# Kernel tuning notes

Measured on AMD Instinct MI355X. Metric: run time of the kernel, lower is better.

Reference implementation:

```python
import jax, jax.numpy as jnp
import numpy as np

D_MODEL = 1024
N_HEADS = 16
D_K = D_MODEL // N_HEADS
D_FF = 4096
EPS = 1e-5


def setup_inputs() -> dict:
    key = jax.random.key(0)
    ks = jax.random.split(key, 12)
    s = 1.0 / np.sqrt(D_MODEL)
    inp = {
        "x": jax.random.normal(ks[0], (2, 2048, D_MODEL), dtype=jnp.float32),
        "Wq": jax.random.normal(ks[1], (D_MODEL, D_MODEL), dtype=jnp.float32) * s,
        "Wk": jax.random.normal(ks[2], (D_MODEL, D_MODEL), dtype=jnp.float32) * s,
        "Wv": jax.random.normal(ks[3], (D_MODEL, D_MODEL), dtype=jnp.float32) * s,
        "Wo": jax.random.normal(ks[4], (D_MODEL, D_MODEL), dtype=jnp.float32) * s,
        "ln1_g": jnp.ones((D_MODEL,), jnp.float32),
        "ln1_b": jnp.zeros((D_MODEL,), jnp.float32),
        "ln2_g": jnp.ones((D_MODEL,), jnp.float32),
        "ln2_b": jnp.zeros((D_MODEL,), jnp.float32),
        "W1": jax.random.normal(ks[5], (D_MODEL, D_FF), dtype=jnp.float32) * s,
        "b1": jnp.zeros((D_FF,), jnp.float32),
        "W2": jax.random.normal(ks[6], (D_FF, D_MODEL), dtype=jnp.float32) * (1.0 / np.sqrt(D_FF)),
        "b2": jnp.zeros((D_MODEL,), jnp.float32),
    }
    return inp


def _layernorm(x, g, b):
    mu = jnp.mean(x, axis=-1, keepdims=True)
    var = jnp.mean(jnp.square(x - mu), axis=-1, keepdims=True)
    return (x - mu) / jnp.sqrt(var + EPS) * g + b


def _mha(x, Wq, Wk, Wv, Wo):
    B, S, D = x.shape
    def split_heads(t):
        return t.reshape(B, S, N_HEADS, D_K).transpose(0, 2, 1, 3)  # [B,H,S,Dk]
    Q = split_heads(x @ Wq)
    K = split_heads(x @ Wk)
    V = split_heads(x @ Wv)
    scores = jnp.einsum("bhsd,bhtd->bhst", Q, K) / np.sqrt(D_K)
    causal = jnp.tril(jnp.ones((S, S), dtype=bool))
    scores = jnp.where(causal, scores, -jnp.inf)
    weights = jax.nn.softmax(scores, axis=-1)
    out = jnp.einsum("bhst,bhtd->bhsd", weights, V)
    out = out.transpose(0, 2, 1, 3).reshape(B, S, D)
    return out @ Wo


def reference(x, Wq, Wk, Wv, Wo, ln1_g, ln1_b, ln2_g, ln2_b, W1, b1, W2, b2):
    # Pre-LN transformer block, dropout in eval mode (identity)
    x = x + _mha(_layernorm(x, ln1_g, ln1_b), Wq, Wk, Wv, Wo)
    h = _layernorm(x, ln2_g, ln2_b)
    ff = jax.nn.gelu(h @ W1 + b1, approximate=False) @ W2 + b2
    return x + ff
```

## Files before the change

kernel.cpp:

```cpp
#include <hip/hip_runtime.h>
#include <cstdint>
#include <cstddef>

#define DEV __device__ __forceinline__

typedef __attribute__((ext_vector_type(8))) __bf16 bf16x8;
typedef __attribute__((ext_vector_type(4))) float f32x4;

typedef const __attribute__((address_space(1))) void gld_gv;
typedef __attribute__((address_space(3))) void gld_sv;

static constexpr int SEQ = 2048, BAT = 2, DM = 1024, DFF = 4096;
static constexpr int MT = BAT * SEQ;
static constexpr float LOG2E = 1.44269504088896340736f;
static constexpr float SM_SHIFT = 16.0f;

struct TrueC  { static constexpr bool value = true;  };
struct FalseC { static constexpr bool value = false; };

DEV unsigned short f2bf_bits(float f) {
    uint32_t u = __builtin_bit_cast(uint32_t, f);
    return (unsigned short)((u + 0x7FFFu + ((u >> 16) & 1u)) >> 16);
}

DEV void gload16(const void* g, void* s) {
    __builtin_amdgcn_global_load_lds((gld_gv*)g, (gld_sv*)s, 16, 0, 0);
}

__global__ __launch_bounds__(256) void wtrans_kernel(const float* __restrict__ W,
        unsigned short* __restrict__ WT, int K, int N, float scale)
{
    __shared__ float tile[64][65];
    const int k0 = blockIdx.x * 64, n0 = blockIdx.y * 64;
    const int t = threadIdx.x, r = t >> 6, c = t & 63;
    #pragma unroll
    for (int p = 0; p < 16; ++p)
        tile[p * 4 + r][c] = W[(size_t)(k0 + p * 4 + r) * N + n0 + c];
    __syncthreads();
    #pragma unroll
    for (int p = 0; p < 16; ++p)
        WT[(size_t)(n0 + p * 4 + r) * K + k0 + c] = f2bf_bits(tile[c][p * 4 + r] * scale);
}

__global__ __launch_bounds__(256) void ln_kernel(const float* __restrict__ x,
        const float* __restrict__ gw, const float* __restrict__ bw,
        unsigned short* __restrict__ y)
{
    const int row = blockIdx.x, t = threadIdx.x;
    const float* xr = x + (size_t)row * DM;
    float4 v = *(const float4*)(xr + t * 4);
    float s = v.x + v.y + v.z + v.w;
    float q = v.x * v.x + v.y * v.y + v.z * v.z + v.w * v.w;
    #pragma unroll
    for (int m = 1; m < 64; m <<= 1) { s += __shfl_xor(s, m); q += __shfl_xor(q, m); }
    __shared__ float red[8];
    const int w = t >> 6;
    if ((t & 63) == 0) { red[w] = s; red[4 + w] = q; }
    __syncthreads();
    s = red[0] + red[1] + red[2] + red[3];
    q = red[4] + red[5] + red[6] + red[7];
    const float mu = s * (1.0f / DM);
    const float rstd = rsqrtf(q * (1.0f / DM) - mu * mu + 1e-5f);
    float4 g4 = *(const float4*)(gw + t * 4);
    float4 b4 = *(const float4*)(bw + t * 4);
    short4 o;
    o.x = (short)f2bf_bits((v.x - mu) * rstd * g4.x + b4.x);
    o.y = (short)f2bf_bits((v.y - mu) * rstd * g4.y + b4.y);
    o.z = (short)f2bf_bits((v.z - mu) * rstd * g4.z + b4.z);
    o.w = (short)f2bf_bits((v.w - mu) * rstd * g4.w + b4.w);
    *(short4*)(y + (size_t)row * DM + t * 4) = o;
}

template<int EPI, int BM, int BN, int WVM, int WVN>
__global__ __launch_bounds__(WVM * WVN * 64, (BN == 64 ? 3 : 2)) void gemm_pipe(
    const unsigned short* __restrict__ A, const unsigned short* __restrict__ BT,
    void* __restrict__ Cp, const float* __restrict__ bias,
    const float* __restrict__ res, int Nsz, int Ksz, float scale)
{
    constexpr int NT = WVM * WVN * 64;
    constexpr int TOTCH = (BM + BN) * 8;
    constexpr int TL = TOTCH / NT;
    constexpr int MREP = BM / (WVM * 16);
    constexpr int WMR = MREP * 16;
    __shared__ alignas(16) unsigned short lds[2][(BM + BN) * 64];

    const int t = threadIdx.x, l = t & 63, w = t >> 6;
    const int wm = w / WVN, wn = w % WVN;
    const int lr = l & 15, lg = l >> 4;
    const int bm = blockIdx.x, bn = blockIdx.y;

    f32x4 acc[MREP][4] = {};

    const int nk = Ksz / 64;

    auto STAGE = [&](int tile, char* slot) {
        const int k0 = tile * 64;
        #pragma unroll
        for (int p = 0; p < TL; ++p) {
            const int ci = t + p * NT;
            const bool isA = ci < BM * 8;
            const int rr = (isA ? ci : ci - BM * 8) >> 3;
            const int cc = ci & 7;
            const unsigned short* srow = isA
                ? A + (size_t)(bm * BM + rr) * Ksz
                : BT + (size_t)(bn * BN + rr) * Ksz;
            gload16(srow + k0 + ((cc ^ (rr & 7)) << 3), slot + ci * 16);
        }
    };

    STAGE(0, (char*)lds[0]);
    STAGE(1, (char*)lds[1]);

    for (int kt = 0; kt < nk; ++kt) {
        char* slot = (char*)lds[kt & 1];
        const char* la = slot;
        const char* lb = slot + BM * 128;
        if (kt + 1 < nk) {
            if constexpr (TL == 8) asm volatile("s_waitcnt vmcnt(8)" ::: "memory");
            else                   asm volatile("s_waitcnt vmcnt(6)" ::: "memory");
        } else {
            asm volatile("s_waitcnt vmcnt(0)" ::: "memory");
        }
        __builtin_amdgcn_s_barrier();
        __builtin_amdgcn_sched_barrier(0);

        __builtin_amdgcn_s_setprio(1);
        #pragma unroll
        for (int ks = 0; ks < 2; ++ks) {
            bf16x8 af[MREP], bfr[4];
            #pragma unroll
            for (int i = 0; i < MREP; ++i) {
                const int ra = wm * WMR + i * 16 + lr;
                af[i] = *(const bf16x8*)(la + (ra * 8 + ((ks * 4 + lg) ^ (ra & 7))) * 16);
            }
            #pragma unroll
            for (int i = 0; i < 4; ++i) {
                const int rb_ = wn * 64 + i * 16 + lr;
                bfr[i] = *(const bf16x8*)(lb + (rb_ * 8 + ((ks * 4 + lg) ^ (rb_ & 7))) * 16);
            }
            #pragma unroll
            for (int mb = 0; mb < MREP; ++mb)
                #pragma unroll
                for (int nb = 0; nb < 4; ++nb) {
                    if (EPI == 4)
                        acc[mb][nb] = __builtin_amdgcn_mfma_f32_16x16x32_bf16(
                            bfr[nb], af[mb], acc[mb][nb], 0, 0, 0);
                    else
                        acc[mb][nb] = __builtin_amdgcn_mfma_f32_16x16x32_bf16(
                            af[mb], bfr[nb], acc[mb][nb], 0, 0, 0);
                }
        }
        __builtin_amdgcn_s_setprio(0);
        __builtin_amdgcn_s_barrier();
        if (kt + 2 < nk) STAGE(kt + 2, slot);
    }

    const int rb = bm * BM + wm * WMR, cb = bn * BN + wn * 64;
    #pragma unroll
    for (int mb = 0; mb < MREP; ++mb)
        #pragma unroll
        for (int nb = 0; nb < 4; ++nb)
            #pragma unroll
            for (int r = 0; r < 4; ++r) {
                float v = acc[mb][nb][r];
                if (EPI == 4) {
                    const int xrow = rb + mb * 16 + lr;
                    const int feat = cb + nb * 16 + lg * 4 + r;
                    const int bb = xrow >> 11, sl = xrow & (SEQ - 1);
                    const int hh = feat >> 6, n = feat & 63;
                    const int nbf = n >> 4, lrf = n & 15;
                    const int ksg = sl >> 5, lgf = (sl & 15) >> 2;
                    const int half = (sl >> 4) & 1, j = sl & 3;
                    ((unsigned short*)Cp)[((size_t)(bb * 16 + hh) * 256 + ksg * 4 + nbf) * 512
                        + (lgf * 16 + lrf) * 8 + half * 4 + j] = f2bf_bits(v);
                    continue;
                }
                const int row = rb + mb * 16 + lg * 4 + r;
                const int col = cb + nb * 16 + lr;
                if (EPI == 5) {
                    if (col < 1024) {
                        ((unsigned short*)Cp)[(size_t)row * 1024 + col] = f2bf_bits(v);
                    } else {
                        const int bb = row >> 11, sl = row & (SEQ - 1);
                        const int hh = (col >> 6) & 15, d = col & 63;
                        const int ktf = sl >> 7, mbf = (sl & 127) >> 4, lrf = sl & 15;
                        const int ksf = d >> 5, lgf = (d & 31) >> 3, j2 = d & 7;
                        unsigned short* Kf = (unsigned short*)(uintptr_t)bias;
                        Kf[((((size_t)(bb * 16 + hh) * 16 + ktf) * 8 + mbf) * 2 + ksf) * 512
                           + (lgf * 16 + lrf) * 8 + j2] = f2bf_bits(v);
                    }
                    continue;
                }
                const size_t idx = (size_t)row * Nsz + col;
                if (EPI == 0) {
                    ((unsigned short*)Cp)[idx] = f2bf_bits(v * scale);
                } else if (EPI == 1) {
                    ((float*)Cp)[idx] = v + res[idx];
                } else if (EPI == 2) {
                    float xx = v + bias[col];
                    ((unsigned short*)Cp)[idx] =
                        f2bf_bits(0.5f * xx * (1.0f + erff(xx * 0.70710678118654752f)));
                } else {
                    ((float*)Cp)[idx] = v + bias[col] + res[idx];
                }
            }
}

template<int P>
DEV void phase8_mfma(const char* base, int wm, int lr, int lg,
                     const bf16x8 (&bfr)[2][4], f32x4 (&acc)[8][4]) {
    bf16x8 af[2][2];
    #pragma unroll
    for (int ks = 0; ks < 2; ++ks)
        #pragma unroll
        for (int m = 0; m < 2; ++m) {
            const int ra = wm * 128 + P * 32 + m * 16 + lr;
            af[ks][m] = *(const bf16x8*)(base + (ra * 8 + ((ks * 4 + lg) ^ (ra & 7))) * 16);
        }
    __builtin_amdgcn_s_barrier();
    __builtin_amdgcn_s_setprio(1);
    #pragma unroll
    for (int ks = 0; ks < 2; ++ks)
        #pragma unroll
        for (int m = 0; m < 2; ++m)
            #pragma unroll
            for (int nb = 0; nb < 4; ++nb)
                acc[P * 2 + m][nb] = __builtin_amdgcn_mfma_f32_16x16x32_bf16(
                    af[ks][m], bfr[ks][nb], acc[P * 2 + m][nb], 0, 0, 0);
    __builtin_amdgcn_s_setprio(0);
}

template<int EPI>
__global__ __launch_bounds__(512, 2) void gemm_8ph(
    const unsigned short* __restrict__ A, const unsigned short* __restrict__ BT,
    void* __restrict__ Cp, const float* __restrict__ bias,
    const float* __restrict__ res, int Nsz, int Ksz, float scale)
{
    __shared__ alignas(16) unsigned short lds[2][32768];
    const int t = threadIdx.x, l = t & 63, w = t >> 6;
    const int wm = w >> 2, wn = w & 3;
    const int lr = l & 15, lg = l >> 4;
    const int bm = blockIdx.x, bn = blockIdx.y;

    f32x4 acc[8][4] = {};
    const int nk = Ksz / 64;

    const unsigned short* Ab = A + (size_t)(bm * 256) * Ksz;
    const unsigned short* Bb = BT + (size_t)(bn * 256) * Ksz;

    auto stage = [&](int tile, int region) {
        char* base = (char*)lds[tile & 1];
        const int k0 = tile * 64;
        #pragma unroll
        for (int j = 0; j < 2; ++j) {
            const int ci = t + j * 512;
            const int rr = ci >> 3, c = ci & 7;
            int row; const unsigned short* src; int dchunk;
            if (region == 0)      { row = rr;                          src = Bb; dchunk = 2048 + row * 8 + c; }
            else if (region == 1) { row = 128 + rr;                    src = Bb; dchunk = 2048 + row * 8 + c; }
            else if (region == 2) { row = (rr < 64 ? rr : rr + 64);    src = Ab; dchunk = row * 8 + c; }
            else                  { row = 64 + (rr < 64 ? rr : rr + 64); src = Ab; dchunk = row * 8 + c; }
            gload16(src + (size_t)row * Ksz + k0 + ((c ^ (row & 7)) << 3),
                    base + dchunk * 16);
        }
    };

    stage(0, 0); stage(0, 1); stage(0, 2); stage(0, 3);
    stage(1, 0); stage(1, 1); stage(1, 2);
    asm volatile("s_waitcnt vmcnt(6)" ::: "memory");
    __builtin_amdgcn_s_barrier();
    __builtin_amdgcn_sched_barrier(0);

    bf16x8 bfr[2][4];
    for (int kt = 0; kt < nk; ++kt) {
        const char* base = (const char*)lds[kt & 1];
        if (kt + 1 < nk) stage(kt + 1, 3);
        #pragma unroll
        for (int ks = 0; ks < 2; ++ks)
            #pragma unroll
            for (int nb = 0; nb < 4; ++nb) {
                const int rb_ = wn * 64 + nb * 16 + lr;
                bfr[ks][nb] = *(const bf16x8*)(base
                    + (2048 + rb_ * 8 + ((ks * 4 + lg) ^ (rb_ & 7))) * 16);
            }
        phase8_mfma<0>(base, wm, lr, lg, bfr, acc);
        __builtin_amdgcn_s_barrier();
        if (kt + 2 < nk) stage(kt + 2, 0);
        phase8_mfma<1>(base, wm, lr, lg, bfr, acc);
        __builtin_amdgcn_s_barrier();
        if (kt + 2 < nk) stage(kt + 2, 1);
        phase8_mfma<2>(base, wm, lr, lg, bfr, acc);
        __builtin_amdgcn_s_barrier();
        if (kt + 2 < nk) stage(kt + 2, 2);
        phase8_mfma<3>(base, wm, lr, lg, bfr, acc);
        if (kt + 2 < nk) asm volatile("s_waitcnt vmcnt(6)" ::: "memory");
        else             asm volatile("s_waitcnt vmcnt(0)" ::: "memory");
        __builtin_amdgcn_s_barrier();
        __builtin_amdgcn_sched_barrier(0);
    }

    const int rb = bm * 256 + wm * 128, cb = bn * 256 + wn * 64;
    #pragma unroll
    for (int mb = 0; mb < 8; ++mb)
        #pragma unroll
        for (int nb = 0; nb < 4; ++nb)
            #pragma unroll
            for (int r = 0; r < 4; ++r) {
                float v = acc[mb][nb][r];
                const int row = rb + mb * 16 + lg * 4 + r;
                const int col = cb + nb * 16 + lr;
                const size_t idx = (size_t)row * Nsz + col;
                if (EPI == 2) {
                    const float xx = v + bias[col];
                    const float tq = xx * xx;
                    const float u = xx * fmaf(tq, 0.044715f, 1.0f);
                    const float e = exp2f(u * -2.30220795f);
                    ((unsigned short*)Cp)[idx] =
                        f2bf_bits(xx * __builtin_amdgcn_rcpf(1.0f + e));
                } else if (EPI == 0) {
                    ((unsigned short*)Cp)[idx] = f2bf_bits(v * scale);
                } else {
                    ((float*)Cp)[idx] = v + bias[col] + res[idx];
                }
            }
}

__global__ __launch_bounds__(512, 2) void attn_kernel(
    const unsigned short* __restrict__ Qg, const unsigned short* __restrict__ Kfg,
    const unsigned short* __restrict__ Vfg, unsigned short* __restrict__ Og)
{
    __shared__ alignas(16) unsigned short ldsK[2][128 * 64];
    __shared__ alignas(16) unsigned short ldsVT[2][64 * 128];
    const int t = threadIdx.x, l = t & 63, w = t >> 6;
    const int lr = l & 15, lg = l >> 4;
    const int qtA = blockIdx.x, qtB = 15 - qtA;
    const int bh = blockIdx.y;
    const int b = bh >> 4, h = bh & 15;
    const unsigned short* Qbase = Qg + (size_t)b * SEQ * 1024 + h * 64;
    const unsigned short* Kbase = Kfg + (size_t)bh * 131072;
    const unsigned short* Vbase = Vfg + (size_t)bh * 131072;

    const int wq0A = qtA * 128 + w * 16, qrowA = wq0A + lr;
    const int wq0B = qtB * 128 + w * 16, qrowB = wq0B + lr;
    bf16x8 qfA[2], qfB[2];
    #pragma unroll
    for (int ks = 0; ks < 2; ++ks) {
        qfA[ks] = *(const bf16x8*)(Qbase + (size_t)qrowA * 1024 + ks * 32 + lg * 8);
        qfB[ks] = *(const bf16x8*)(Qbase + (size_t)qrowB * 1024 + ks * 32 + lg * 8);
    }

    f32x4 oaccA[4] = {}, oaccB[4] = {};
    f32x4 laccA = {}, laccB = {};
    bf16x8 onesv;
    #pragma unroll
    for (int i = 0; i < 8; ++i) onesv[i] = (__bf16)1.0f;

    const int lby = l * 16;
    const int nkt = qtB + 1;

    #pragma unroll
    for (int p = 0; p < 2; ++p) {
        const int ci = t + p * 512;
        gload16(Kbase + (size_t)ci * 8, (char*)ldsK[0] + ci * 16);
        gload16(Vbase + (size_t)ci * 8, (char*)ldsVT[0] + ci * 16);
    }
    asm volatile("s_waitcnt vmcnt(0)" ::: "memory");
    __builtin_amdgcn_s_barrier();

    for (int kt = 0; kt < nkt; ++kt) {
        const int cur = kt & 1;
        if (kt + 1 < nkt) {
            #pragma unroll
            for (int p = 0; p < 2; ++p) {
                const int ci = t + p * 512;
                gload16(Kbase + (size_t)((kt + 1) * 1024 + ci) * 8,
                        (char*)ldsK[cur ^ 1] + ci * 16);
                gload16(Vbase + (size_t)((kt + 1) * 1024 + ci) * 8,
                        (char*)ldsVT[cur ^ 1] + ci * 16);
            }
            asm volatile("s_waitcnt vmcnt(4)" ::: "memory");
        } else {
            asm volatile("s_waitcnt vmcnt(0)" ::: "memory");
        }
        __builtin_amdgcn_s_barrier();
        __builtin_amdgcn_sched_barrier(0);

        const char* lk = (const char*)ldsK[cur];
        const char* lv = (const char*)ldsVT[cur];
        const int kt0 = kt * 128;

        auto run_softmax = [&](f32x4 (&st)[8], int qrow, bool diag, bf16x8 (&pa)[4]) {
            if (diag) {
                #pragma unroll
                for (int mb = 0; mb < 8; ++mb)
                    #pragma unroll
                    for (int r = 0; r < 4; ++r)
                        if (kt0 + mb * 16 + lg * 4 + r > qrow) st[mb][r] = -1e30f;
            }
            #pragma unroll
            for (int mb = 0; mb < 8; ++mb)
                #pragma unroll
                for (int r = 0; r < 4; ++r)
                    st[mb][r] = exp2f(st[mb][r]);
            #pragma unroll
            for (int ks = 0; ks < 4; ++ks)
                #pragma unroll
                for (int j = 0; j < 4; ++j) {
                    pa[ks][j]     = (__bf16)st[2 * ks][j];
                    pa[ks][j + 4] = (__bf16)st[2 * ks + 1][j];
                }
        };

        auto iter_body = [&](auto DOA) {
            constexpr bool doA = DOA.value;
            f32x4 stA[8], stB[8];
            #pragma unroll
            for (int mb = 0; mb < 8; ++mb)
                #pragma unroll
                for (int r = 0; r < 4; ++r) { stA[mb][r] = -SM_SHIFT; stB[mb][r] = -SM_SHIFT; }
            __builtin_amdgcn_s_setprio(1);
            #pragma unroll
            for (int ks = 0; ks < 2; ++ks)
                #pragma unroll
                for (int mb = 0; mb < 8; ++mb) {
                    bf16x8 kf = *(const bf16x8*)(lk + (mb * 2 + ks) * 1024 + lby);
                    if constexpr (doA)
                        stA[mb] = __builtin_amdgcn_mfma_f32_16x16x32_bf16(kf, qfA[ks], stA[mb], 0, 0, 0);
                    stB[mb] = __builtin_amdgcn_mfma_f32_16x16x32_bf16(kf, qfB[ks], stB[mb], 0, 0, 0);
                }
            __builtin_amdgcn_s_setprio(0);

            bf16x8 paA[4], paB[4];
            if constexpr (doA)
                run_softmax(stA, qrowA, kt == qtA, paA);
            run_softmax(stB, qrowB, kt == qtB, paB);

            __builtin_amdgcn_s_setprio(1);
            #pragma unroll
            for (int ks = 0; ks < 4; ++ks) {
                #pragma unroll
                for (int nb = 0; nb < 4; ++nb) {
                    bf16x8 vbv = *(const bf16x8*)(lv + (ks * 4 + nb) * 1024 + lby);
                    if constexpr (doA)
                        oaccA[nb] = __builtin_amdgcn_mfma_f32_16x16x32_bf16(paA[ks], vbv, oaccA[nb], 0, 0, 0);
                    oaccB[nb] = __builtin_amdgcn_mfma_f32_16x16x32_bf16(paB[ks], vbv, oaccB[nb], 0, 0, 0);
                }
                if constexpr (doA)
                    laccA = __builtin_amdgcn_mfma_f32_16x16x32_bf16(paA[ks], onesv, laccA, 0, 0, 0);
                laccB = __builtin_amdgcn_mfma_f32_16x16x32_bf16(paB[ks], onesv, laccB, 0, 0, 0);
            }
            __builtin_amdgcn_s_setprio(0);
        };

        if (kt <= qtA) iter_body(TrueC{}); else iter_body(FalseC{});

        __builtin_amdgcn_s_barrier();
    }

    unsigned short* Obase = Og + (size_t)b * SEQ * DM + h * 64;
    #pragma unroll
    for (int j = 0; j < 4; ++j) {
        const float invA = 1.0f / laccA[j];
        const float invB = 1.0f / laccB[j];
        const int rowA = wq0A + lg * 4 + j;
        const int rowB = wq0B + lg * 4 + j;
        #pragma unroll
        for (int nb = 0; nb < 4; ++nb) {
            Obase[(size_t)rowA * DM + nb * 16 + lr] = f2bf_bits(oaccA[nb][j] * invA);
            Obase[(size_t)rowB * DM + nb * 16 + lr] = f2bf_bits(oaccB[nb][j] * invB);
        }
    }
}

extern "C" void kernel_launch(void* const* d_in, const int* in_sizes, int n_in,
                              void* d_out, int out_size, void* d_ws, size_t ws_size,
                              hipStream_t stream) {
    (void)in_sizes; (void)n_in; (void)out_size; (void)ws_size;
    const float* x    = (const float*)d_in[0];
    const float* Wq   = (const float*)d_in[1];
    const float* Wk   = (const float*)d_in[2];
    const float* Wv   = (const float*)d_in[3];
    const float* Wo   = (const float*)d_in[4];
    const float* ln1g = (const float*)d_in[5];
    const float* ln1b = (const float*)d_in[6];
    const float* ln2g = (const float*)d_in[7];
    const float* ln2b = (const float*)d_in[8];
    const float* W1   = (const float*)d_in[9];
    const float* b1   = (const float*)d_in[10];
    const float* W2   = (const float*)d_in[11];
    const float* b2   = (const float*)d_in[12];
    float* out = (float*)d_out;

    char* ws = (char*)d_ws;
    const size_t MB = 1ull << 20;
    unsigned short* xn1   = (unsigned short*)(ws + 0 * MB);
    unsigned short* Qb    = (unsigned short*)(ws + 8 * MB);
    unsigned short* Kf    = (unsigned short*)(ws + 16 * MB);
    unsigned short* Vf    = (unsigned short*)(ws + 24 * MB);
    unsigned short* ffa   = (unsigned short*)(ws + 0 * MB);
    unsigned short* attno = (unsigned short*)(ws + 32 * MB);
    float*          x2    = (float*)(ws + 40 * MB);
    unsigned short* h2    = (unsigned short*)(ws + 56 * MB);
    unsigned short* WqkT  = (unsigned short*)(ws + 64 * MB);
    unsigned short* WvT   = (unsigned short*)(ws + 68 * MB);
    unsigned short* WoT   = (unsigned short*)(ws + 70 * MB);
    unsigned short* W1T   = (unsigned short*)(ws + 72 * MB);
    unsigned short* W2T   = (unsigned short*)(ws + 80 * MB);

    dim3 blk(256);
    wtrans_kernel<<<dim3(16, 16), blk, 0, stream>>>(Wq, WqkT, DM, DM, 0.125f * LOG2E);
    wtrans_kernel<<<dim3(16, 16), blk, 0, stream>>>(Wk, WqkT + DM * DM, DM, DM, 1.0f);
    wtrans_kernel<<<dim3(16, 16), blk, 0, stream>>>(Wv, WvT, DM, DM, 1.0f);
    wtrans_kernel<<<dim3(16, 16), blk, 0, stream>>>(Wo, WoT, DM, DM, 1.0f);
    wtrans_kernel<<<dim3(16, 64), blk, 0, stream>>>(W1, W1T, DM, DFF, 1.0f);
    wtrans_kernel<<<dim3(64, 16), blk, 0, stream>>>(W2, W2T, DFF, DM, 1.0f);

    ln_kernel<<<dim3(MT), blk, 0, stream>>>(x, ln1g, ln1b, xn1);

    gemm_pipe<5, 128, 256, 2, 4><<<dim3(32, 8), dim3(512), 0, stream>>>(
        xn1, WqkT, Qb, (const float*)Kf, nullptr, 2048, DM, 1.0f);
    gemm_pipe<4, 128, 64, 4, 1><<<dim3(32, 16), blk, 0, stream>>>(
        xn1, WvT, Vf, nullptr, nullptr, DM, DM, 1.0f);

    attn_kernel<<<dim3(8, 32), dim3(512), 0, stream>>>(Qb, Kf, Vf, attno);

    gemm_pipe<1, 128, 64, 4, 1><<<dim3(32, 16), blk, 0, stream>>>(
        attno, WoT, x2, nullptr, x, DM, DM, 1.0f);

    ln_kernel<<<dim3(MT), blk, 0, stream>>>(x2, ln2g, ln2b, h2);

    gemm_8ph<2><<<dim3(16, 16), dim3(512), 0, stream>>>(
        h2, W1T, ffa, b1, nullptr, DFF, DM, 1.0f);
    gemm_pipe<3, 128, 64, 4, 1><<<dim3(32, 16), blk, 0, stream>>>(
        ffa, W2T, out, b2, x2, DM, DFF, 1.0f);
}
```

Baseline: 227.2 us.

## Fuse weight transposes into one launch and shrink attention tiles to 64

The six weight-transpose launches become a single kernel that picks its source matrix from the block index, which cuts launch overhead. The attention kernel moves from 512-thread blocks with 128-row query and key tiles to 256-thread blocks with 64-row tiles. That doubles the grid to 512 blocks while keeping the paired-tile causal balancing. More, smaller blocks should fill the CUs better and shorten the causal tail, at the cost of more K/V reloads and more barriers per key token.

```diff
diff --git a/kernel.cpp b/kernel.cpp
--- a/kernel.cpp
+++ b/kernel.cpp
@@ -27,11 +27,24 @@
     __builtin_amdgcn_global_load_lds((gld_gv*)g, (gld_sv*)s, 16, 0, 0);
 }
 
-__global__ __launch_bounds__(256) void wtrans_kernel(const float* __restrict__ W,
-        unsigned short* __restrict__ WT, int K, int N, float scale)
+__global__ __launch_bounds__(256) void wtrans_all(
+    const float* __restrict__ Wq, const float* __restrict__ Wk,
+    const float* __restrict__ Wv, const float* __restrict__ Wo,
+    const float* __restrict__ W1, const float* __restrict__ W2,
+    unsigned short* __restrict__ WqkT, unsigned short* __restrict__ WvT,
+    unsigned short* __restrict__ WoT, unsigned short* __restrict__ W1T,
+    unsigned short* __restrict__ W2T)
 {
+    const int id = blockIdx.x;
+    const float* W; unsigned short* WT; int K, N, k0, n0; float scale = 1.0f;
+    if (id < 256)       { int loc = id;        W = Wq; WT = WqkT;             K = 1024; N = 1024; k0 = (loc & 15) * 64; n0 = (loc >> 4) * 64; scale = 0.125f * LOG2E; }
+    else if (id < 512)  { int loc = id - 256;  W = Wk; WT = WqkT + 1024*1024; K = 1024; N = 1024; k0 = (loc & 15) * 64; n0 = (loc >> 4) * 64; }
+    else if (id < 768)  { int loc = id - 512;  W = Wv; WT = WvT;              K = 1024; N = 1024; k0 = (loc & 15) * 64; n0 = (loc >> 4) * 64; }
+    else if (id < 1024) { int loc = id - 768;  W = Wo; WT = WoT;              K = 1024; N = 1024; k0 = (loc & 15) * 64; n0 = (loc >> 4) * 64; }
+    else if (id < 2048) { int loc = id - 1024; W = W1; WT = W1T;              K = 1024; N = 4096; k0 = (loc & 15) * 64; n0 = (loc >> 4) * 64; }
+    else                { int loc = id - 2048; W = W2; WT = W2T;              K = 4096; N = 1024; k0 = (loc & 63) * 64; n0 = (loc >> 6) * 64; }
+
     __shared__ float tile[64][65];
-    const int k0 = blockIdx.x * 64, n0 = blockIdx.y * 64;
     const int t = threadIdx.x, r = t >> 6, c = t & 63;
     #pragma unroll
     for (int p = 0; p < 16; ++p)
@@ -325,23 +338,23 @@
             }
 }
 
-__global__ __launch_bounds__(512, 2) void attn_kernel(
+__global__ __launch_bounds__(256, 4) void attn_kernel(
     const unsigned short* __restrict__ Qg, const unsigned short* __restrict__ Kfg,
     const unsigned short* __restrict__ Vfg, unsigned short* __restrict__ Og)
 {
-    __shared__ alignas(16) unsigned short ldsK[2][128 * 64];
-    __shared__ alignas(16) unsigned short ldsVT[2][64 * 128];
+    __shared__ alignas(16) unsigned short ldsK[2][64 * 64];
+    __shared__ alignas(16) unsigned short ldsVT[2][64 * 64];
     const int t = threadIdx.x, l = t & 63, w = t >> 6;
     const int lr = l & 15, lg = l >> 4;
-    const int qtA = blockIdx.x, qtB = 15 - qtA;
+    const int qA = blockIdx.x, qB = 31 - qA;
     const int bh = blockIdx.y;
     const int b = bh >> 4, h = bh & 15;
     const unsigned short* Qbase = Qg + (size_t)b * SEQ * 1024 + h * 64;
     const unsigned short* Kbase = Kfg + (size_t)bh * 131072;
     const unsigned short* Vbase = Vfg + (size_t)bh * 131072;
 
-    const int wq0A = qtA * 128 + w * 16, qrowA = wq0A + lr;
-    const int wq0B = qtB * 128 + w * 16, qrowB = wq0B + lr;
+    const int wq0A = qA * 64 + w * 16, qrowA = wq0A + lr;
+    const int wq0B = qB * 64 + w * 16, qrowB = wq0B + lr;
     bf16x8 qfA[2], qfB[2];
     #pragma unroll
     for (int ks = 0; ks < 2; ++ks) {
@@ -356,11 +369,11 @@
     for (int i = 0; i < 8; ++i) onesv[i] = (__bf16)1.0f;
 
     const int lby = l * 16;
-    const int nkt = qtB + 1;
+    const int nkt = qB + 1;
 
     #pragma unroll
     for (int p = 0; p < 2; ++p) {
-        const int ci = t + p * 512;
+        const int ci = t + p * 256;
         gload16(Kbase + (size_t)ci * 8, (char*)ldsK[0] + ci * 16);
         gload16(Vbase + (size_t)ci * 8, (char*)ldsVT[0] + ci * 16);
     }
@@ -372,10 +385,10 @@
         if (kt + 1 < nkt) {
             #pragma unroll
             for (int p = 0; p < 2; ++p) {
-                const int ci = t + p * 512;
-                gload16(Kbase + (size_t)((kt + 1) * 1024 + ci) * 8,
+                const int ci = t + p * 256;
+                gload16(Kbase + (size_t)((kt + 1) * 512 + ci) * 8,
                         (char*)ldsK[cur ^ 1] + ci * 16);
-                gload16(Vbase + (size_t)((kt + 1) * 1024 + ci) * 8,
+                gload16(Vbase + (size_t)((kt + 1) * 512 + ci) * 8,
                         (char*)ldsVT[cur ^ 1] + ci * 16);
             }
             asm volatile("s_waitcnt vmcnt(4)" ::: "memory");
@@ -387,23 +400,23 @@
 
         const char* lk = (const char*)ldsK[cur];
         const char* lv = (const char*)ldsVT[cur];
-        const int kt0 = kt * 128;
-
-        auto run_softmax = [&](f32x4 (&st)[8], int qrow, bool diag, bf16x8 (&pa)[4]) {
+        const int kt0 = kt * 64;
+
+        auto run_softmax = [&](f32x4 (&st)[4], int qrow, bool diag, bf16x8 (&pa)[2]) {
             if (diag) {
                 #pragma unroll
-                for (int mb = 0; mb < 8; ++mb)
+                for (int mb = 0; mb < 4; ++mb)
                     #pragma unroll
                     for (int r = 0; r < 4; ++r)
                         if (kt0 + mb * 16 + lg * 4 + r > qrow) st[mb][r] = -1e30f;
             }
             #pragma unroll
-            for (int mb = 0; mb < 8; ++mb)
+            for (int mb = 0; mb < 4; ++mb)
                 #pragma unroll
                 for (int r = 0; r < 4; ++r)
                     st[mb][r] = exp2f(st[mb][r]);
             #pragma unroll
-            for (int ks = 0; ks < 4; ++ks)
+            for (int ks = 0; ks < 2; ++ks)
                 #pragma unroll
                 for (int j = 0; j < 4; ++j) {
                     pa[ks][j]     = (__bf16)st[2 * ks][j];
@@ -413,16 +426,16 @@
 
         auto iter_body = [&](auto DOA) {
             constexpr bool doA = DOA.value;
-            f32x4 stA[8], stB[8];
-            #pragma unroll
-            for (int mb = 0; mb < 8; ++mb)
+            f32x4 stA[4], stB[4];
+            #pragma unroll
+            for (int mb = 0; mb < 4; ++mb)
                 #pragma unroll
                 for (int r = 0; r < 4; ++r) { stA[mb][r] = -SM_SHIFT; stB[mb][r] = -SM_SHIFT; }
             __builtin_amdgcn_s_setprio(1);
             #pragma unroll
             for (int ks = 0; ks < 2; ++ks)
                 #pragma unroll
-                for (int mb = 0; mb < 8; ++mb) {
+                for (int mb = 0; mb < 4; ++mb) {
                     bf16x8 kf = *(const bf16x8*)(lk + (mb * 2 + ks) * 1024 + lby);
                     if constexpr (doA)
                         stA[mb] = __builtin_amdgcn_mfma_f32_16x16x32_bf16(kf, qfA[ks], stA[mb], 0, 0, 0);
@@ -430,14 +443,14 @@
                 }
             __builtin_amdgcn_s_setprio(0);
 
-            bf16x8 paA[4], paB[4];
+            bf16x8 paA[2], paB[2];
             if constexpr (doA)
-                run_softmax(stA, qrowA, kt == qtA, paA);
-            run_softmax(stB, qrowB, kt == qtB, paB);
+                run_softmax(stA, qrowA, kt == qA, paA);
+            run_softmax(stB, qrowB, kt == qB, paB);
 
             __builtin_amdgcn_s_setprio(1);
             #pragma unroll
-            for (int ks = 0; ks < 4; ++ks) {
+            for (int ks = 0; ks < 2; ++ks) {
                 #pragma unroll
                 for (int nb = 0; nb < 4; ++nb) {
                     bf16x8 vbv = *(const bf16x8*)(lv + (ks * 4 + nb) * 1024 + lby);
@@ -452,7 +465,7 @@
             __builtin_amdgcn_s_setprio(0);
         };
 
-        if (kt <= qtA) iter_body(TrueC{}); else iter_body(FalseC{});
+        if (kt <= qA) iter_body(TrueC{}); else iter_body(FalseC{});
 
         __builtin_amdgcn_s_barrier();
     }
@@ -508,12 +521,8 @@
     unsigned short* W2T   = (unsigned short*)(ws + 80 * MB);
 
     dim3 blk(256);
-    wtrans_kernel<<<dim3(16, 16), blk, 0, stream>>>(Wq, WqkT, DM, DM, 0.125f * LOG2E);
-    wtrans_kernel<<<dim3(16, 16), blk, 0, stream>>>(Wk, WqkT + DM * DM, DM, DM, 1.0f);
-    wtrans_kernel<<<dim3(16, 16), blk, 0, stream>>>(Wv, WvT, DM, DM, 1.0f);
-    wtrans_kernel<<<dim3(16, 16), blk, 0, stream>>>(Wo, WoT, DM, DM, 1.0f);
-    wtrans_kernel<<<dim3(16, 64), blk, 0, stream>>>(W1, W1T, DM, DFF, 1.0f);
-    wtrans_kernel<<<dim3(64, 16), blk, 0, stream>>>(W2, W2T, DFF, DM, 1.0f);
+    wtrans_all<<<dim3(3072), blk, 0, stream>>>(Wq, Wk, Wv, Wo, W1, W2,
+                                               WqkT, WvT, WoT, W1T, W2T);
 
     ln_kernel<<<dim3(MT), blk, 0, stream>>>(x, ln1g, ln1b, xn1);
 
@@ -522,7 +531,7 @@
     gemm_pipe<4, 128, 64, 4, 1><<<dim3(32, 16), blk, 0, stream>>>(
         xn1, WvT, Vf, nullptr, nullptr, DM, DM, 1.0f);
 
-    attn_kernel<<<dim3(8, 32), dim3(512), 0, stream>>>(Qb, Kf, Vf, attno);
+    attn_kernel<<<dim3(16, 32), blk, 0, stream>>>(Qb, Kf, Vf, attno);
 
     gemm_pipe<1, 128, 64, 4, 1><<<dim3(32, 16), blk, 0, stream>>>(
         attno, WoT, x2, nullptr, x, DM, DM, 1.0f);
```

Result: faster. 216.8 us (-4.6%).
